# Optimization experiments

Hardware: AMD Instinct MI355X
Metric: run time of the kernel (lower is better)

Reference implementation:

```python
import jax, jax.numpy as jnp
import numpy as np

EMBED_DIM = 1024
NUM_HEADS = 16
HEAD_DIM = EMBED_DIM // NUM_HEADS


def setup_inputs() -> dict:
    key = jax.random.key(0)
    k1, k2, k3, k4, k5 = jax.random.split(key, 5)
    B, S, D = 2, 2048, EMBED_DIM
    s_in = 1.0 / np.sqrt(D)
    x = jax.random.normal(k1, (B, S, D), dtype=jnp.float32)
    W_qkv = jax.random.uniform(k2, (D, 3 * D), dtype=jnp.float32, minval=-s_in, maxval=s_in)
    b_qkv = jax.random.uniform(k3, (3 * D,), dtype=jnp.float32, minval=-s_in, maxval=s_in)
    W_out = jax.random.uniform(k4, (D, D), dtype=jnp.float32, minval=-s_in, maxval=s_in)
    b_out = jax.random.uniform(k5, (D,), dtype=jnp.float32, minval=-s_in, maxval=s_in)
    return {"x": x, "W_qkv": W_qkv, "b_qkv": b_qkv, "W_out": W_out, "b_out": b_out}


def reference(x, W_qkv, b_qkv, W_out, b_out):
    B, S, D = x.shape
    H, Hd = NUM_HEADS, HEAD_DIM
    qkv = x @ W_qkv + b_qkv                      # [B,S,3D]
    qkv = qkv.reshape(B, S, 3, H, Hd)
    q = qkv[:, :, 0].transpose(0, 2, 1, 3)       # [B,H,S,Hd]
    k = qkv[:, :, 1].transpose(0, 2, 1, 3)
    v = qkv[:, :, 2].transpose(0, 2, 1, 3)
    scores = jnp.einsum('bhsd,bhtd->bhst', q, k) / jnp.sqrt(jnp.float32(Hd))
    attn = jax.nn.softmax(scores, axis=-1)       # dropout is identity in eval mode
    out = jnp.einsum('bhst,bhtd->bhsd', attn, v)
    out = out.transpose(0, 2, 1, 3).reshape(B, S, D)
    return out @ W_out + b_out
```

## Files before the change

### kernel.cpp

```cpp
#include <hip/hip_runtime.h>
#include <stdint.h>
#include <math.h>

#define EMBED 1024
#define HEADS 16
#define HDIM  64
#define SEQ   2048
#define BATCH 2

typedef __bf16 bf16x8 __attribute__((ext_vector_type(8)));
typedef float  f32x4  __attribute__((ext_vector_type(4)));
typedef unsigned short u16x8 __attribute__((ext_vector_type(8)));
typedef unsigned short u16x4 __attribute__((ext_vector_type(4)));
typedef uint32_t u32x4v __attribute__((ext_vector_type(4)));

static __device__ __forceinline__ unsigned short f2bf(float f){
  union { float f; uint32_t u; } v; v.f = f;
  uint32_t u = v.u;
  uint32_t r = (u + 0x7FFFu + ((u >> 16) & 1u)) >> 16;
  return (unsigned short)r;
}
static __device__ __forceinline__ bf16x8 as_bf(u16x8 v){ return __builtin_bit_cast(bf16x8, v); }

static __device__ __forceinline__ uint32_t pk_bf16(float a, float b){
#if defined(__has_builtin) && __has_builtin(__builtin_amdgcn_cvt_pk_bf16_f32)
  typedef __bf16 bf16x2 __attribute__((ext_vector_type(2)));
  bf16x2 p = __builtin_amdgcn_cvt_pk_bf16_f32(a, b);
  return __builtin_bit_cast(uint32_t, p);
#else
  return (uint32_t)f2bf(a) | ((uint32_t)f2bf(b) << 16);
#endif
}

static __device__ __forceinline__ float fexp2(float x){
#if defined(__has_builtin) && __has_builtin(__builtin_amdgcn_exp2f)
  return __builtin_amdgcn_exp2f(x);
#else
  return exp2f(x);
#endif
}

static __device__ __forceinline__ void stage16(const unsigned short* gp,
                                               unsigned short* lp_wave, int lane){
#if defined(__has_builtin) && __has_builtin(__builtin_amdgcn_global_load_lds)
  __builtin_amdgcn_global_load_lds((const __attribute__((address_space(1))) void*)gp,
                                   (__attribute__((address_space(3))) void*)lp_wave,
                                   16, 0, 0);
#else
  *(u16x8*)(lp_wave + lane * 8) = *(const u16x8*)gp;
#endif
}

__global__ __launch_bounds__(256) void prep(
    const float* __restrict__ x,      unsigned short* __restrict__ xb,
    const float* __restrict__ W_qkv,  unsigned short* __restrict__ wqkvT,
    const float* __restrict__ W_out,  unsigned short* __restrict__ woutT)
{
  __shared__ unsigned short T[32 * 36];
  const int bid = blockIdx.x;
  const int t   = threadIdx.x;

  if (bid < 4096){
    int i = (bid * 256 + t) * 4;
    float4 v = *(const float4*)(x + i);
    u16x4 o;
    o[0] = f2bf(v.x); o[1] = f2bf(v.y); o[2] = f2bf(v.z); o[3] = f2bf(v.w);
    *(u16x4*)(xb + i) = o;
    return;
  }
  const float* W; unsigned short* Wt; int N, n0, k0;
  if (bid < 7168){
    int idx = bid - 4096;
    W = W_qkv; Wt = wqkvT; N = 3072;
    n0 = (idx % 96) * 32; k0 = (idx / 96) * 32;
  } else {
    int idx = bid - 7168;
    W = W_out; Wt = woutT; N = 1024;
    n0 = (idx & 31) * 32; k0 = (idx >> 5) * 32;
  }
  int kr = t >> 3, nc = (t & 7) * 4;
  float4 wv = *(const float4*)(W + (size_t)(k0 + kr) * N + n0 + nc);
  T[(nc + 0) * 36 + kr] = f2bf(wv.x);
  T[(nc + 1) * 36 + kr] = f2bf(wv.y);
  T[(nc + 2) * 36 + kr] = f2bf(wv.z);
  T[(nc + 3) * 36 + kr] = f2bf(wv.w);
  __syncthreads();
  int nr = t >> 3, kc = (t & 7) * 4;
  *(u16x4*)(Wt + (size_t)(n0 + nr) * 1024 + k0 + kc) = *(const u16x4*)&T[nr * 36 + kc];
}

__global__ __launch_bounds__(256) void vtrans(const unsigned short* __restrict__ V,
                                              unsigned short* __restrict__ VT){
  __shared__ unsigned short T[32 * 36];
  int t = threadIdx.x;
  int s0 = blockIdx.x * 32, d0 = blockIdx.y * 32;
  size_t base = (size_t)blockIdx.z * SEQ * HDIM;
  int sr = t >> 3, dc = (t & 7) * 4;
  u16x4 vv = *(const u16x4*)(V + base + (size_t)(s0 + sr) * HDIM + d0 + dc);
  T[(dc + 0) * 36 + sr] = vv[0];
  T[(dc + 1) * 36 + sr] = vv[1];
  T[(dc + 2) * 36 + sr] = vv[2];
  T[(dc + 3) * 36 + sr] = vv[3];
  __syncthreads();
  int dr = t >> 3, sc = (t & 7) * 4;
  int pos = (((sc >> 2) & 3) << 3) + (((sc >> 4) & 1) << 2);
  *(u16x4*)(VT + base + (size_t)(d0 + dr) * SEQ + s0 + pos) = *(const u16x4*)&T[dr * 36 + sc];
}

__global__ __launch_bounds__(256) void gemm_qkv(
    const unsigned short* __restrict__ A,
    const unsigned short* __restrict__ Bt,
    const float* __restrict__ bias,
    unsigned short* __restrict__ q_ws,
    unsigned short* __restrict__ k_ws,
    unsigned short* __restrict__ v_ws,
    int M, int N, int K)
{
  __shared__ unsigned short As[128 * 64];
  __shared__ unsigned short Bs[128 * 64];
  const int tid  = threadIdx.x;
  const int bm   = blockIdx.x, bn = blockIdx.y;
  const int w    = tid >> 6, lane = tid & 63;
  const int quad = lane >> 4, l16 = lane & 15;
  const int wm   = (w >> 1) * 64, wn = (w & 1) * 64;

  f32x4 acc[4][4] = {};

  for (int k0 = 0; k0 < K; k0 += 64) {
    #pragma unroll
    for (int i = 0; i < 4; i++){
      int c = w * 4 + i;
      int row = c * 8 + (lane >> 3);
      int kg = (lane & 7) ^ (row & 7);
      stage16(A  + (size_t)(bm * 128 + row) * K + k0 + kg * 8, &As[c * 512], lane);
      stage16(Bt + (size_t)(bn * 128 + row) * K + k0 + kg * 8, &Bs[c * 512], lane);
    }
    __syncthreads();

    #pragma unroll
    for (int kk = 0; kk < 2; kk++){
      bf16x8 af[4], bfr[4];
      #pragma unroll
      for (int t = 0; t < 4; t++){
        int ra = wm + t * 16 + l16;
        int rb = wn + t * 16 + l16;
        af[t]  = as_bf(*(const u16x8*)&As[(ra << 6) + ((((kk << 2) + quad) ^ (ra & 7)) << 3)]);
        bfr[t] = as_bf(*(const u16x8*)&Bs[(rb << 6) + ((((kk << 2) + quad) ^ (rb & 7)) << 3)]);
      }
      #pragma unroll
      for (int mt = 0; mt < 4; mt++)
        #pragma unroll
        for (int nt = 0; nt < 4; nt++)
          acc[mt][nt] = __builtin_amdgcn_mfma_f32_16x16x32_bf16(af[mt], bfr[nt], acc[mt][nt], 0, 0, 0);
    }
    __syncthreads();
  }

  const int which = (bn * 128) >> 10;
  unsigned short* dst = (which == 0) ? q_ws : (which == 1) ? k_ws : v_ws;
  const float scale = (which == 0) ? 0.18033688f : 1.0f;
  const int b = bm >> 4;
  #pragma unroll
  for (int nt = 0; nt < 4; nt++){
    int gnb = bn * 128 + wn + nt * 16;
    int h   = (gnb & 1023) >> 6;
    int hd  = (gnb & 63) + l16;
    float bv = bias[gnb + l16];
    unsigned short* dp = dst + (size_t)(b * HEADS + h) * SEQ * HDIM + hd;
    #pragma unroll
    for (int mt = 0; mt < 4; mt++){
      int s0 = ((bm & 15) * 128) + wm + mt * 16 + quad * 4;
      #pragma unroll
      for (int r = 0; r < 4; r++)
        dp[(size_t)(s0 + r) * HDIM] = f2bf((acc[mt][nt][r] + bv) * scale);
    }
  }
}

__global__ __launch_bounds__(256) void gemm_out(
    const unsigned short* __restrict__ A,
    const unsigned short* __restrict__ Bt,
    const float* __restrict__ bias,
    float* __restrict__ Cout,
    int M, int N, int K)
{
  __shared__ unsigned short As[128 * 64];
  __shared__ unsigned short Bs[64 * 64];
  const int tid  = threadIdx.x;
  const int bm   = blockIdx.x, bn = blockIdx.y;
  const int w    = tid >> 6, lane = tid & 63;
  const int quad = lane >> 4, l16 = lane & 15;
  const int wm   = (w >> 1) * 64, wn = (w & 1) * 32;

  f32x4 acc[4][2] = {};

  for (int k0 = 0; k0 < K; k0 += 64) {
    #pragma unroll
    for (int i = 0; i < 4; i++){
      int c = w * 4 + i;
      int row = c * 8 + (lane >> 3);
      int kg = (lane & 7) ^ (row & 7);
      stage16(A + (size_t)(bm * 128 + row) * K + k0 + kg * 8, &As[c * 512], lane);
    }
    #pragma unroll
    for (int i = 0; i < 2; i++){
      int c = w * 2 + i;
      int row = c * 8 + (lane >> 3);
      int kg = (lane & 7) ^ (row & 7);
      stage16(Bt + (size_t)(bn * 64 + row) * K + k0 + kg * 8, &Bs[c * 512], lane);
    }
    __syncthreads();

    #pragma unroll
    for (int kk = 0; kk < 2; kk++){
      bf16x8 af[4], bfr[2];
      #pragma unroll
      for (int t = 0; t < 4; t++){
        int ra = wm + t * 16 + l16;
        af[t] = as_bf(*(const u16x8*)&As[(ra << 6) + ((((kk << 2) + quad) ^ (ra & 7)) << 3)]);
      }
      #pragma unroll
      for (int t = 0; t < 2; t++){
        int rb = wn + t * 16 + l16;
        bfr[t] = as_bf(*(const u16x8*)&Bs[(rb << 6) + ((((kk << 2) + quad) ^ (rb & 7)) << 3)]);
      }
      #pragma unroll
      for (int mt = 0; mt < 4; mt++)
        #pragma unroll
        for (int nt = 0; nt < 2; nt++)
          acc[mt][nt] = __builtin_amdgcn_mfma_f32_16x16x32_bf16(af[mt], bfr[nt], acc[mt][nt], 0, 0, 0);
    }
    __syncthreads();
  }

  #pragma unroll
  for (int mt = 0; mt < 4; mt++)
    #pragma unroll
    for (int nt = 0; nt < 2; nt++)
      #pragma unroll
      for (int r = 0; r < 4; r++){
        int gm = bm * 128 + wm + mt * 16 + quad * 4 + r;
        int gn = bn * 64 + wn + nt * 16 + l16;
        Cout[(size_t)gm * N + gn] = acc[mt][nt][r] + bias[gn];
      }
}

__global__ __launch_bounds__(512) void attn(
    const unsigned short* __restrict__ q_ws,
    const unsigned short* __restrict__ k_ws,
    const unsigned short* __restrict__ vt_ws,
    unsigned short* __restrict__ o_ws)
{
  __shared__ unsigned short Qs[256 * 64];
  __shared__ unsigned short Ks[2][64 * 64];
  __shared__ unsigned short VTs[2][64 * 64];
  const int tid  = threadIdx.x;
  const int wgid = blockIdx.x;
  const int lin  = (wgid & 7) * 32 + (wgid >> 3);
  const int bh   = lin >> 3, qt = lin & 7;
  const int w    = tid >> 6, lane = tid & 63;
  const int quad = lane >> 4, l16 = lane & 15;
  const size_t base = (size_t)bh * SEQ * HDIM;

  #pragma unroll
  for (int i = 0; i < 4; i++){
    int c = w * 4 + i;
    int row = c * 8 + (lane >> 3);
    int kg = (lane & 7) ^ (row & 7);
    stage16(q_ws + base + (size_t)(qt * 256 + row) * HDIM + kg * 8, &Qs[c * 512], lane);
  }

  const int srow = w * 8 + (lane >> 3);
  const int skg  = (lane & 7) ^ (srow & 7);
  const int dofs = w * 512 + lane * 8;

  stage16(k_ws  + base + (size_t)srow * HDIM + skg * 8, &Ks[0][w * 512],  lane);
  stage16(vt_ws + base + (size_t)srow * SEQ + skg * 8,  &VTs[0][w * 512], lane);
  __syncthreads();

  bf16x8 bq[2][2];
  #pragma unroll
  for (int mq = 0; mq < 2; mq++){
    int row = w * 32 + mq * 16 + l16;
    #pragma unroll
    for (int ks = 0; ks < 2; ks++)
      bq[mq][ks] = as_bf(*(const u16x8*)&Qs[(row << 6) + ((((ks << 2) + quad) ^ (row & 7)) << 3)]);
  }

  const unsigned short* kp = k_ws  + base + (size_t)(64 + srow) * HDIM + skg * 8;
  const unsigned short* vp = vt_ws + base + (size_t)srow * SEQ + 64 + skg * 8;

  f32x4 acc[2][4] = {};
  float li[2] = {0.f, 0.f};

  for (int kt2 = 0; kt2 < SEQ / 128; kt2++){
    #pragma unroll
    for (int half = 0; half < 2; half++){
      const int cur = half;
      const int kt  = kt2 * 2 + half;
      u16x8 kpre, vpre;
      if (kt < SEQ / 64 - 1){
        kpre = *(const u16x8*)kp;  kp += 64 * HDIM;
        vpre = *(const u16x8*)vp;  vp += 64;
      }

      f32x4 sf[4][2] = {};
      #pragma unroll
      for (int ks = 0; ks < 2; ks++){
        #pragma unroll
        for (int nt = 0; nt < 4; nt++){
          int rk = nt * 16 + l16;
          bf16x8 ak = as_bf(*(const u16x8*)&Ks[cur][(rk << 6) + ((((ks << 2) + quad) ^ (rk & 7)) << 3)]);
          #pragma unroll
          for (int mq = 0; mq < 2; mq++)
            sf[nt][mq] = __builtin_amdgcn_mfma_f32_16x16x32_bf16(ak, bq[mq][ks], sf[nt][mq], 0, 0, 0);
        }
      }

      #pragma unroll
      for (int nt = 0; nt < 4; nt++)
        #pragma unroll
        for (int mq = 0; mq < 2; mq++)
          #pragma unroll
          for (int r = 0; r < 4; r++)
            sf[nt][mq][r] = fexp2(sf[nt][mq][r]);
      #pragma unroll
      for (int mq = 0; mq < 2; mq++)
        #pragma unroll
        for (int nt = 0; nt < 4; nt++)
          li[mq] += (sf[nt][mq][0] + sf[nt][mq][1]) + (sf[nt][mq][2] + sf[nt][mq][3]);

      #pragma unroll
      for (int c = 0; c < 2; c++){
        bf16x8 ap[2];
        #pragma unroll
        for (int mq = 0; mq < 2; mq++){
          u32x4v aw;
          aw[0] = pk_bf16(sf[c * 2][mq][0],     sf[c * 2][mq][1]);
          aw[1] = pk_bf16(sf[c * 2][mq][2],     sf[c * 2][mq][3]);
          aw[2] = pk_bf16(sf[c * 2 + 1][mq][0], sf[c * 2 + 1][mq][1]);
          aw[3] = pk_bf16(sf[c * 2 + 1][mq][2], sf[c * 2 + 1][mq][3]);
          ap[mq] = __builtin_bit_cast(bf16x8, aw);
        }
        #pragma unroll
        for (int nt = 0; nt < 4; nt++){
          int rv = nt * 16 + l16;
          bf16x8 bv = as_bf(*(const u16x8*)&VTs[cur][(rv << 6) + ((((c << 2) + quad) ^ (rv & 7)) << 3)]);
          #pragma unroll
          for (int mq = 0; mq < 2; mq++)
            acc[mq][nt] = __builtin_amdgcn_mfma_f32_16x16x32_bf16(ap[mq], bv, acc[mq][nt], 0, 0, 0);
        }
      }

      if (kt < SEQ / 64 - 1){
        *(u16x8*)&Ks[cur ^ 1][dofs]  = kpre;
        *(u16x8*)&VTs[cur ^ 1][dofs] = vpre;
      }
      __syncthreads();
    }
  }

  #pragma unroll
  for (int mq = 0; mq < 2; mq++){
    li[mq] += __shfl_xor(li[mq], 16);
    li[mq] += __shfl_xor(li[mq], 32);
  }
  float inv[2] = {1.0f / li[0], 1.0f / li[1]};
  float invr[2][4];
  #pragma unroll
  for (int mq = 0; mq < 2; mq++)
    #pragma unroll
    for (int r = 0; r < 4; r++)
      invr[mq][r] = __shfl(inv[mq], quad * 4 + r);

  int b = bh >> 4, h = bh & 15;
  #pragma unroll
  for (int mq = 0; mq < 2; mq++)
    #pragma unroll
    for (int nt = 0; nt < 4; nt++)
      #pragma unroll
      for (int r = 0; r < 4; r++){
        int s = qt * 256 + w * 32 + mq * 16 + quad * 4 + r;
        int d = h * 64 + nt * 16 + l16;
        o_ws[((size_t)(b * SEQ + s)) * EMBED + d] = f2bf(acc[mq][nt][r] * invr[mq][r]);
      }
}

extern "C" void kernel_launch(void* const* d_in, const int* in_sizes, int n_in,
                              void* d_out, int out_size, void* d_ws, size_t ws_size,
                              hipStream_t stream) {
  const float* x     = (const float*)d_in[0];
  const float* W_qkv = (const float*)d_in[1];
  const float* b_qkv = (const float*)d_in[2];
  const float* W_out = (const float*)d_in[3];
  const float* b_out = (const float*)d_in[4];
  float* out = (float*)d_out;

  char* ws = (char*)d_ws;
  unsigned short* xb    = (unsigned short*)(ws);
  unsigned short* vt    = (unsigned short*)(ws);
  unsigned short* q     = (unsigned short*)(ws + ((size_t)8  << 20));
  unsigned short* k     = (unsigned short*)(ws + ((size_t)16 << 20));
  unsigned short* v     = (unsigned short*)(ws + ((size_t)24 << 20));
  unsigned short* o     = (unsigned short*)(ws + ((size_t)24 << 20));
  unsigned short* wqkvT = (unsigned short*)(ws + ((size_t)32 << 20));
  unsigned short* woutT = (unsigned short*)(ws + ((size_t)38 << 20));

  prep<<<dim3(8192), dim3(256), 0, stream>>>(x, xb, W_qkv, wqkvT, W_out, woutT);

  gemm_qkv<<<dim3(32, 24), dim3(256), 0, stream>>>(
      xb, wqkvT, b_qkv, q, k, v, 4096, 3072, 1024);

  vtrans<<<dim3(64, 2, 32), dim3(256), 0, stream>>>(v, vt);

  attn<<<dim3(256), dim3(512), 0, stream>>>(q, k, vt, o);

  gemm_out<<<dim3(32, 16), dim3(256), 0, stream>>>(
      o, woutT, b_out, out, 4096, 1024, 1024);
}
```

Baseline: 197.5 us.

## Fuse V transpose into QKV GEMM epilogue and split attention KV across two groups

The QKV GEMM epilogue now writes V directly in transposed, permuted layout, which removes the separate vtrans kernel launch and one round trip of V through memory. The attention kernel changes to 128-query tiles with two 256-thread groups, each covering half of the key sequence, and doubles the grid to 512 blocks. The groups merge their partial accumulators and row sums through shared memory at the end, which works because the softmax uses no running max. This adds more parallelism for a small grid, in exchange for an extra LDS reduction and strided transposed V stores in the GEMM epilogue.

```diff
diff --git a/kernel.cpp b/kernel.cpp
--- a/kernel.cpp
+++ b/kernel.cpp
@@ -89,31 +89,13 @@
   *(u16x4*)(Wt + (size_t)(n0 + nr) * 1024 + k0 + kc) = *(const u16x4*)&T[nr * 36 + kc];
 }
 
-__global__ __launch_bounds__(256) void vtrans(const unsigned short* __restrict__ V,
-                                              unsigned short* __restrict__ VT){
-  __shared__ unsigned short T[32 * 36];
-  int t = threadIdx.x;
-  int s0 = blockIdx.x * 32, d0 = blockIdx.y * 32;
-  size_t base = (size_t)blockIdx.z * SEQ * HDIM;
-  int sr = t >> 3, dc = (t & 7) * 4;
-  u16x4 vv = *(const u16x4*)(V + base + (size_t)(s0 + sr) * HDIM + d0 + dc);
-  T[(dc + 0) * 36 + sr] = vv[0];
-  T[(dc + 1) * 36 + sr] = vv[1];
-  T[(dc + 2) * 36 + sr] = vv[2];
-  T[(dc + 3) * 36 + sr] = vv[3];
-  __syncthreads();
-  int dr = t >> 3, sc = (t & 7) * 4;
-  int pos = (((sc >> 2) & 3) << 3) + (((sc >> 4) & 1) << 2);
-  *(u16x4*)(VT + base + (size_t)(d0 + dr) * SEQ + s0 + pos) = *(const u16x4*)&T[dr * 36 + sc];
-}
-
 __global__ __launch_bounds__(256) void gemm_qkv(
     const unsigned short* __restrict__ A,
     const unsigned short* __restrict__ Bt,
     const float* __restrict__ bias,
     unsigned short* __restrict__ q_ws,
     unsigned short* __restrict__ k_ws,
-    unsigned short* __restrict__ v_ws,
+    unsigned short* __restrict__ vt_ws,
     int M, int N, int K)
 {
   __shared__ unsigned short As[128 * 64];
@@ -157,9 +139,31 @@
   }
 
   const int which = (bn * 128) >> 10;
-  unsigned short* dst = (which == 0) ? q_ws : (which == 1) ? k_ws : v_ws;
+  const int b = bm >> 4;
+  const int S_base = (bm & 15) * 128 + wm;
+
+  if (which == 2){
+    #pragma unroll
+    for (int nt = 0; nt < 4; nt++){
+      int gnb = bn * 128 + wn + nt * 16;
+      int h   = (gnb & 1023) >> 6;
+      int d   = (gnb & 63) + l16;
+      float bv = bias[gnb + l16];
+      unsigned short* vp = vt_ws + (size_t)(b * HEADS + h) * SEQ * HDIM + (size_t)d * SEQ;
+      #pragma unroll
+      for (int mt = 0; mt < 4; mt++){
+        int spos = S_base + (mt >> 1) * 32 + quad * 8 + (mt & 1) * 4;
+        u16x4 o4;
+        #pragma unroll
+        for (int r = 0; r < 4; r++) o4[r] = f2bf(acc[mt][nt][r] + bv);
+        *(u16x4*)(vp + spos) = o4;
+      }
+    }
+    return;
+  }
+
+  unsigned short* dst = (which == 0) ? q_ws : k_ws;
   const float scale = (which == 0) ? 0.18033688f : 1.0f;
-  const int b = bm >> 4;
   #pragma unroll
   for (int nt = 0; nt < 4; nt++){
     int gnb = bn * 128 + wn + nt * 16;
@@ -169,7 +173,7 @@
     unsigned short* dp = dst + (size_t)(b * HEADS + h) * SEQ * HDIM + hd;
     #pragma unroll
     for (int mt = 0; mt < 4; mt++){
-      int s0 = ((bm & 15) * 128) + wm + mt * 16 + quad * 4;
+      int s0 = S_base + mt * 16 + quad * 4;
       #pragma unroll
       for (int r = 0; r < 4; r++)
         dp[(size_t)(s0 + r) * HDIM] = f2bf((acc[mt][nt][r] + bv) * scale);
@@ -251,114 +255,139 @@
     const unsigned short* __restrict__ vt_ws,
     unsigned short* __restrict__ o_ws)
 {
-  __shared__ unsigned short Qs[256 * 64];
-  __shared__ unsigned short Ks[2][64 * 64];
-  __shared__ unsigned short VTs[2][64 * 64];
+  __shared__ unsigned short SM[32768];
   const int tid  = threadIdx.x;
   const int wgid = blockIdx.x;
-  const int lin  = (wgid & 7) * 32 + (wgid >> 3);
-  const int bh   = lin >> 3, qt = lin & 7;
-  const int w    = tid >> 6, lane = tid & 63;
+  const int lin  = (wgid & 7) * 64 + (wgid >> 3);
+  const int bh   = lin >> 4, qt = lin & 15;
+  const int grp  = tid >> 8;
+  const int w    = (tid >> 6) & 3, lane = tid & 63;
   const int quad = lane >> 4, l16 = lane & 15;
   const size_t base = (size_t)bh * SEQ * HDIM;
-
-  #pragma unroll
-  for (int i = 0; i < 4; i++){
-    int c = w * 4 + i;
-    int row = c * 8 + (lane >> 3);
-    int kg = (lane & 7) ^ (row & 7);
-    stage16(q_ws + base + (size_t)(qt * 256 + row) * HDIM + kg * 8, &Qs[c * 512], lane);
-  }
-
-  const int srow = w * 8 + (lane >> 3);
-  const int skg  = (lane & 7) ^ (srow & 7);
-  const int dofs = w * 512 + lane * 8;
-
-  stage16(k_ws  + base + (size_t)srow * HDIM + skg * 8, &Ks[0][w * 512],  lane);
-  stage16(vt_ws + base + (size_t)srow * SEQ + skg * 8,  &VTs[0][w * 512], lane);
+  unsigned short* Ks  = SM + grp * 16384;
+  unsigned short* VTs = Ks + 8192;
+  const int kvb = grp * 1024;
+
+  bf16x8 bq[2][2];
+  #pragma unroll
+  for (int mq = 0; mq < 2; mq++){
+    int qrow = qt * 128 + w * 32 + mq * 16 + l16;
+    #pragma unroll
+    for (int ks = 0; ks < 2; ks++)
+      bq[mq][ks] = as_bf(*(const u16x8*)(q_ws + base + (size_t)qrow * HDIM + (ks * 4 + quad) * 8));
+  }
+
+  const int row0 = w * 16 + (lane >> 3), row1 = row0 + 8;
+  const int kg0 = (lane & 7) ^ (row0 & 7), kg1 = (lane & 7) ^ (row1 & 7);
+  const int dofs0 = (w * 2) * 512 + lane * 8, dofs1 = dofs0 + 512;
+
+  stage16(k_ws  + base + (size_t)(kvb + row0) * HDIM + kg0 * 8, Ks  + (w * 2) * 512,     lane);
+  stage16(k_ws  + base + (size_t)(kvb + row1) * HDIM + kg1 * 8, Ks  + (w * 2 + 1) * 512, lane);
+  stage16(vt_ws + base + (size_t)row0 * SEQ + kvb + kg0 * 8,    VTs + (w * 2) * 512,     lane);
+  stage16(vt_ws + base + (size_t)row1 * SEQ + kvb + kg1 * 8,    VTs + (w * 2 + 1) * 512, lane);
   __syncthreads();
 
-  bf16x8 bq[2][2];
-  #pragma unroll
-  for (int mq = 0; mq < 2; mq++){
-    int row = w * 32 + mq * 16 + l16;
-    #pragma unroll
-    for (int ks = 0; ks < 2; ks++)
-      bq[mq][ks] = as_bf(*(const u16x8*)&Qs[(row << 6) + ((((ks << 2) + quad) ^ (row & 7)) << 3)]);
-  }
-
-  const unsigned short* kp = k_ws  + base + (size_t)(64 + srow) * HDIM + skg * 8;
-  const unsigned short* vp = vt_ws + base + (size_t)srow * SEQ + 64 + skg * 8;
+  const unsigned short* kp0 = k_ws  + base + (size_t)(kvb + 64 + row0) * HDIM + kg0 * 8;
+  const unsigned short* kp1 = k_ws  + base + (size_t)(kvb + 64 + row1) * HDIM + kg1 * 8;
+  const unsigned short* vp0 = vt_ws + base + (size_t)row0 * SEQ + kvb + 64 + kg0 * 8;
+  const unsigned short* vp1 = vt_ws + base + (size_t)row1 * SEQ + kvb + 64 + kg1 * 8;
 
   f32x4 acc[2][4] = {};
   float li[2] = {0.f, 0.f};
 
-  for (int kt2 = 0; kt2 < SEQ / 128; kt2++){
-    #pragma unroll
-    for (int half = 0; half < 2; half++){
-      const int cur = half;
-      const int kt  = kt2 * 2 + half;
-      u16x8 kpre, vpre;
-      if (kt < SEQ / 64 - 1){
-        kpre = *(const u16x8*)kp;  kp += 64 * HDIM;
-        vpre = *(const u16x8*)vp;  vp += 64;
-      }
-
-      f32x4 sf[4][2] = {};
-      #pragma unroll
-      for (int ks = 0; ks < 2; ks++){
-        #pragma unroll
-        for (int nt = 0; nt < 4; nt++){
-          int rk = nt * 16 + l16;
-          bf16x8 ak = as_bf(*(const u16x8*)&Ks[cur][(rk << 6) + ((((ks << 2) + quad) ^ (rk & 7)) << 3)]);
-          #pragma unroll
-          for (int mq = 0; mq < 2; mq++)
-            sf[nt][mq] = __builtin_amdgcn_mfma_f32_16x16x32_bf16(ak, bq[mq][ks], sf[nt][mq], 0, 0, 0);
-        }
-      }
-
+  for (int kt = 0; kt < 16; kt++){
+    const int co = (kt & 1) * 4096;
+    u16x8 kpre0, kpre1, vpre0, vpre1;
+    if (kt < 15){
+      kpre0 = *(const u16x8*)kp0;  kp0 += 64 * HDIM;
+      kpre1 = *(const u16x8*)kp1;  kp1 += 64 * HDIM;
+      vpre0 = *(const u16x8*)vp0;  vp0 += 64;
+      vpre1 = *(const u16x8*)vp1;  vp1 += 64;
+    }
+
+    f32x4 sf[4][2] = {};
+    #pragma unroll
+    for (int ks = 0; ks < 2; ks++)
+      #pragma unroll
+      for (int nt = 0; nt < 4; nt++){
+        int rk = nt * 16 + l16;
+        bf16x8 ak = as_bf(*(const u16x8*)&Ks[co + (rk << 6) + ((((ks << 2) + quad) ^ (rk & 7)) << 3)]);
+        #pragma unroll
+        for (int mq = 0; mq < 2; mq++)
+          sf[nt][mq] = __builtin_amdgcn_mfma_f32_16x16x32_bf16(ak, bq[mq][ks], sf[nt][mq], 0, 0, 0);
+      }
+
+    #pragma unroll
+    for (int nt = 0; nt < 4; nt++)
+      #pragma unroll
+      for (int mq = 0; mq < 2; mq++)
+        #pragma unroll
+        for (int r = 0; r < 4; r++)
+          sf[nt][mq][r] = fexp2(sf[nt][mq][r]);
+    #pragma unroll
+    for (int mq = 0; mq < 2; mq++)
       #pragma unroll
       for (int nt = 0; nt < 4; nt++)
+        li[mq] += (sf[nt][mq][0] + sf[nt][mq][1]) + (sf[nt][mq][2] + sf[nt][mq][3]);
+
+    #pragma unroll
+    for (int c = 0; c < 2; c++){
+      bf16x8 ap[2];
+      #pragma unroll
+      for (int mq = 0; mq < 2; mq++){
+        u32x4v aw;
+        aw[0] = pk_bf16(sf[c * 2][mq][0],     sf[c * 2][mq][1]);
+        aw[1] = pk_bf16(sf[c * 2][mq][2],     sf[c * 2][mq][3]);
+        aw[2] = pk_bf16(sf[c * 2 + 1][mq][0], sf[c * 2 + 1][mq][1]);
+        aw[3] = pk_bf16(sf[c * 2 + 1][mq][2], sf[c * 2 + 1][mq][3]);
+        ap[mq] = __builtin_bit_cast(bf16x8, aw);
+      }
+      #pragma unroll
+      for (int nt = 0; nt < 4; nt++){
+        int rv = nt * 16 + l16;
+        bf16x8 bv = as_bf(*(const u16x8*)&VTs[co + (rv << 6) + ((((c << 2) + quad) ^ (rv & 7)) << 3)]);
         #pragma unroll
         for (int mq = 0; mq < 2; mq++)
-          #pragma unroll
-          for (int r = 0; r < 4; r++)
-            sf[nt][mq][r] = fexp2(sf[nt][mq][r]);
-      #pragma unroll
-      for (int mq = 0; mq < 2; mq++)
-        #pragma unroll
-        for (int nt = 0; nt < 4; nt++)
-          li[mq] += (sf[nt][mq][0] + sf[nt][mq][1]) + (sf[nt][mq][2] + sf[nt][mq][3]);
-
-      #pragma unroll
-      for (int c = 0; c < 2; c++){
-        bf16x8 ap[2];
-        #pragma unroll
-        for (int mq = 0; mq < 2; mq++){
-          u32x4v aw;
-          aw[0] = pk_bf16(sf[c * 2][mq][0],     sf[c * 2][mq][1]);
-          aw[1] = pk_bf16(sf[c * 2][mq][2],     sf[c * 2][mq][3]);
-          aw[2] = pk_bf16(sf[c * 2 + 1][mq][0], sf[c * 2 + 1][mq][1]);
-          aw[3] = pk_bf16(sf[c * 2 + 1][mq][2], sf[c * 2 + 1][mq][3]);
-          ap[mq] = __builtin_bit_cast(bf16x8, aw);
-        }
-        #pragma unroll
-        for (int nt = 0; nt < 4; nt++){
-          int rv = nt * 16 + l16;
-          bf16x8 bv = as_bf(*(const u16x8*)&VTs[cur][(rv << 6) + ((((c << 2) + quad) ^ (rv & 7)) << 3)]);
-          #pragma unroll
-          for (int mq = 0; mq < 2; mq++)
-            acc[mq][nt] = __builtin_amdgcn_mfma_f32_16x16x32_bf16(ap[mq], bv, acc[mq][nt], 0, 0, 0);
-        }
-      }
-
-      if (kt < SEQ / 64 - 1){
-        *(u16x8*)&Ks[cur ^ 1][dofs]  = kpre;
-        *(u16x8*)&VTs[cur ^ 1][dofs] = vpre;
-      }
-      __syncthreads();
-    }
-  }
+          acc[mq][nt] = __builtin_amdgcn_mfma_f32_16x16x32_bf16(ap[mq], bv, acc[mq][nt], 0, 0, 0);
+      }
+    }
+
+    if (kt < 15){
+      const int no = (co ^ 4096);
+      *(u16x8*)&Ks[no + dofs0]  = kpre0;
+      *(u16x8*)&Ks[no + dofs1]  = kpre1;
+      *(u16x8*)&VTs[no + dofs0] = vpre0;
+      *(u16x8*)&VTs[no + dofs1] = vpre1;
+    }
+    __syncthreads();
+  }
+
+  float* CBa = (float*)SM;
+  float* CBl = (float*)(SM + 16384);
+  const int gtid = tid & 255;
+  if (grp == 1){
+    #pragma unroll
+    for (int mq = 0; mq < 2; mq++)
+      #pragma unroll
+      for (int nt = 0; nt < 4; nt++)
+        #pragma unroll
+        for (int r = 0; r < 4; r++)
+          CBa[((mq * 4 + nt) * 4 + r) * 256 + gtid] = acc[mq][nt][r];
+    CBl[gtid]       = li[0];
+    CBl[256 + gtid] = li[1];
+  }
+  __syncthreads();
+  if (grp == 1) return;
+
+  #pragma unroll
+  for (int mq = 0; mq < 2; mq++)
+    #pragma unroll
+    for (int nt = 0; nt < 4; nt++)
+      #pragma unroll
+      for (int r = 0; r < 4; r++)
+        acc[mq][nt][r] += CBa[((mq * 4 + nt) * 4 + r) * 256 + gtid];
+  li[0] += CBl[gtid];
+  li[1] += CBl[256 + gtid];
 
   #pragma unroll
   for (int mq = 0; mq < 2; mq++){
@@ -380,7 +409,7 @@
     for (int nt = 0; nt < 4; nt++)
       #pragma unroll
       for (int r = 0; r < 4; r++){
-        int s = qt * 256 + w * 32 + mq * 16 + quad * 4 + r;
+        int s = qt * 128 + w * 32 + mq * 16 + quad * 4 + r;
         int d = h * 64 + nt * 16 + l16;
         o_ws[((size_t)(b * SEQ + s)) * EMBED + d] = f2bf(acc[mq][nt][r] * invr[mq][r]);
       }
@@ -398,22 +427,19 @@
 
   char* ws = (char*)d_ws;
   unsigned short* xb    = (unsigned short*)(ws);
-  unsigned short* vt    = (unsigned short*)(ws);
+  unsigned short* o     = (unsigned short*)(ws);
   unsigned short* q     = (unsigned short*)(ws + ((size_t)8  << 20));
   unsigned short* k     = (unsigned short*)(ws + ((size_t)16 << 20));
-  unsigned short* v     = (unsigned short*)(ws + ((size_t)24 << 20));
-  unsigned short* o     = (unsigned short*)(ws + ((size_t)24 << 20));
+  unsigned short* vt    = (unsigned short*)(ws + ((size_t)24 << 20));
   unsigned short* wqkvT = (unsigned short*)(ws + ((size_t)32 << 20));
   unsigned short* woutT = (unsigned short*)(ws + ((size_t)38 << 20));
 
   prep<<<dim3(8192), dim3(256), 0, stream>>>(x, xb, W_qkv, wqkvT, W_out, woutT);
 
   gemm_qkv<<<dim3(32, 24), dim3(256), 0, stream>>>(
-      xb, wqkvT, b_qkv, q, k, v, 4096, 3072, 1024);
-
-  vtrans<<<dim3(64, 2, 32), dim3(256), 0, stream>>>(v, vt);
-
-  attn<<<dim3(256), dim3(512), 0, stream>>>(q, k, vt, o);
+      xb, wqkvT, b_qkv, q, k, vt, 4096, 3072, 1024);
+
+  attn<<<dim3(512), dim3(512), 0, stream>>>(q, k, vt, o);
 
   gemm_out<<<dim3(32, 16), dim3(256), 0, stream>>>(
       o, woutT, b_out, out, 4096, 1024, 1024);
```

After: 197.9 us. About the same (+0.2%).

## Fuse V transpose into QKV GEMM epilogue with LDS-staged coalesced stores

Applied to the files above, without the earlier changes.

Removes the separate vtrans kernel. The QKV GEMM now writes V already transposed, with the same permuted sequence ordering, by staging the output tile in shared memory. Q and K outputs are also staged through LDS so global stores become 16-byte vector writes instead of scattered 2-byte stores. This saves a kernel launch and a full write-plus-read round trip of V. In exchange, LDS per block grows slightly and the epilogue gains an extra barrier. The workspace layout changes so the attention output aliases the consumed x buffer.

```diff
diff --git a/kernel.cpp b/kernel.cpp
--- a/kernel.cpp
+++ b/kernel.cpp
@@ -89,35 +89,18 @@
   *(u16x4*)(Wt + (size_t)(n0 + nr) * 1024 + k0 + kc) = *(const u16x4*)&T[nr * 36 + kc];
 }
 
-__global__ __launch_bounds__(256) void vtrans(const unsigned short* __restrict__ V,
-                                              unsigned short* __restrict__ VT){
-  __shared__ unsigned short T[32 * 36];
-  int t = threadIdx.x;
-  int s0 = blockIdx.x * 32, d0 = blockIdx.y * 32;
-  size_t base = (size_t)blockIdx.z * SEQ * HDIM;
-  int sr = t >> 3, dc = (t & 7) * 4;
-  u16x4 vv = *(const u16x4*)(V + base + (size_t)(s0 + sr) * HDIM + d0 + dc);
-  T[(dc + 0) * 36 + sr] = vv[0];
-  T[(dc + 1) * 36 + sr] = vv[1];
-  T[(dc + 2) * 36 + sr] = vv[2];
-  T[(dc + 3) * 36 + sr] = vv[3];
-  __syncthreads();
-  int dr = t >> 3, sc = (t & 7) * 4;
-  int pos = (((sc >> 2) & 3) << 3) + (((sc >> 4) & 1) << 2);
-  *(u16x4*)(VT + base + (size_t)(d0 + dr) * SEQ + s0 + pos) = *(const u16x4*)&T[dr * 36 + sc];
-}
-
 __global__ __launch_bounds__(256) void gemm_qkv(
     const unsigned short* __restrict__ A,
     const unsigned short* __restrict__ Bt,
     const float* __restrict__ bias,
     unsigned short* __restrict__ q_ws,
     unsigned short* __restrict__ k_ws,
-    unsigned short* __restrict__ v_ws,
+    unsigned short* __restrict__ vt_ws,
     int M, int N, int K)
 {
-  __shared__ unsigned short As[128 * 64];
-  __shared__ unsigned short Bs[128 * 64];
+  __shared__ unsigned short SM[128 * 136];
+  unsigned short* As = SM;
+  unsigned short* Bs = SM + 8192;
   const int tid  = threadIdx.x;
   const int bm   = blockIdx.x, bn = blockIdx.y;
   const int w    = tid >> 6, lane = tid & 63;
@@ -132,8 +115,8 @@
       int c = w * 4 + i;
       int row = c * 8 + (lane >> 3);
       int kg = (lane & 7) ^ (row & 7);
-      stage16(A  + (size_t)(bm * 128 + row) * K + k0 + kg * 8, &As[c * 512], lane);
-      stage16(Bt + (size_t)(bn * 128 + row) * K + k0 + kg * 8, &Bs[c * 512], lane);
+      stage16(A  + (size_t)(bm * 128 + row) * K + k0 + kg * 8, As + c * 512, lane);
+      stage16(Bt + (size_t)(bn * 128 + row) * K + k0 + kg * 8, Bs + c * 512, lane);
     }
     __syncthreads();
 
@@ -157,22 +140,59 @@
   }
 
   const int which = (bn * 128) >> 10;
-  unsigned short* dst = (which == 0) ? q_ws : (which == 1) ? k_ws : v_ws;
-  const float scale = (which == 0) ? 0.18033688f : 1.0f;
   const int b = bm >> 4;
-  #pragma unroll
-  for (int nt = 0; nt < 4; nt++){
-    int gnb = bn * 128 + wn + nt * 16;
-    int h   = (gnb & 1023) >> 6;
-    int hd  = (gnb & 63) + l16;
-    float bv = bias[gnb + l16];
-    unsigned short* dp = dst + (size_t)(b * HEADS + h) * SEQ * HDIM + hd;
-    #pragma unroll
-    for (int mt = 0; mt < 4; mt++){
-      int s0 = ((bm & 15) * 128) + wm + mt * 16 + quad * 4;
-      #pragma unroll
-      for (int r = 0; r < 4; r++)
-        dp[(size_t)(s0 + r) * HDIM] = f2bf((acc[mt][nt][r] + bv) * scale);
+  const int S0 = (bm & 15) * 128;
+
+  if (which == 2){
+    #pragma unroll
+    for (int nt = 0; nt < 4; nt++){
+      int coln = wn + nt * 16 + l16;
+      float bv = bias[bn * 128 + coln];
+      #pragma unroll
+      for (int mt = 0; mt < 4; mt++){
+        int sposl = wm + (mt >> 1) * 32 + quad * 8 + (mt & 1) * 4;
+        #pragma unroll
+        for (int r = 0; r < 4; r++)
+          SM[coln * 136 + sposl + r] = f2bf(acc[mt][nt][r] + bv);
+      }
+    }
+  } else {
+    const float scale = (which == 0) ? 0.18033688f : 1.0f;
+    #pragma unroll
+    for (int nt = 0; nt < 4; nt++){
+      int coln = wn + nt * 16 + l16;
+      float bv = bias[bn * 128 + coln];
+      #pragma unroll
+      for (int mt = 0; mt < 4; mt++){
+        int sl = wm + mt * 16 + quad * 4;
+        #pragma unroll
+        for (int r = 0; r < 4; r++)
+          SM[(sl + r) * 136 + coln] = f2bf((acc[mt][nt][r] + bv) * scale);
+      }
+    }
+  }
+  __syncthreads();
+
+  if (which == 2){
+    #pragma unroll
+    for (int p = 0; p < 8; p++){
+      int nl = p * 16 + (tid >> 4);
+      int s0 = (tid & 15) * 8;
+      u16x8 v = *(const u16x8*)&SM[nl * 136 + s0];
+      int ng = bn * 128 + nl;
+      int h = (ng & 1023) >> 6, d = ng & 63;
+      *(u16x8*)(vt_ws + (size_t)(b * HEADS + h) * SEQ * HDIM + (size_t)d * SEQ + S0 + s0) = v;
+    }
+  } else {
+    unsigned short* dst = (which == 0) ? q_ws : k_ws;
+    #pragma unroll
+    for (int p = 0; p < 8; p++){
+      int sl = p * 16 + (tid >> 4);
+      int c0 = (tid & 15) * 8;
+      u16x8 v = *(const u16x8*)&SM[sl * 136 + c0];
+      int ng = bn * 128 + c0;
+      int h = (ng & 1023) >> 6, d = ng & 63;
+      *(u16x8*)(dst + (size_t)(b * HEADS + h) * SEQ * HDIM + (size_t)(S0 + sl) * HDIM + d) = v;
     }
   }
 }
@@ -398,20 +418,17 @@
 
   char* ws = (char*)d_ws;
   unsigned short* xb    = (unsigned short*)(ws);
-  unsigned short* vt    = (unsigned short*)(ws);
+  unsigned short* o     = (unsigned short*)(ws);
   unsigned short* q     = (unsigned short*)(ws + ((size_t)8  << 20));
   unsigned short* k     = (unsigned short*)(ws + ((size_t)16 << 20));
-  unsigned short* v     = (unsigned short*)(ws + ((size_t)24 << 20));
-  unsigned short* o     = (unsigned short*)(ws + ((size_t)24 << 20));
+  unsigned short* vt    = (unsigned short*)(ws + ((size_t)24 << 20));
   unsigned short* wqkvT = (unsigned short*)(ws + ((size_t)32 << 20));
   unsigned short* woutT = (unsigned short*)(ws + ((size_t)38 << 20));
 
   prep<<<dim3(8192), dim3(256), 0, stream>>>(x, xb, W_qkv, wqkvT, W_out, woutT);
 
   gemm_qkv<<<dim3(32, 24), dim3(256), 0, stream>>>(
-      xb, wqkvT, b_qkv, q, k, v, 4096, 3072, 1024);
-
-  vtrans<<<dim3(64, 2, 32), dim3(256), 0, stream>>>(v, vt);
+      xb, wqkvT, b_qkv, q, k, vt, 4096, 3072, 1024);
 
   attn<<<dim3(256), dim3(512), 0, stream>>>(q, k, vt, o);
 
```

Result: faster. 189.4 us (-4.1%).
